# Performance work log

Measured on AMD Instinct MI355X. Metric: run time of the kernel, lower is better.

Reference implementation:

```python
import jax, jax.numpy as jnp
import numpy as np

BN_EPS = 1e-5

def conv1d(x, w, b, pad):
    # x: (B, C_in, L), w: (C_out, C_in, K=4), stride 1
    y = jax.lax.conv_general_dilated(x, w, window_strides=(1,), padding=[(pad, pad)],
                                     dimension_numbers=('NCH', 'OIH', 'NCH'))
    return y + b[None, :, None]

def batchnorm_train(x, g, be):
    # training-mode BN over (N, L) per channel, biased variance (torch semantics)
    m = jnp.mean(x, axis=(0, 2), keepdims=True)
    v = jnp.mean((x - m) ** 2, axis=(0, 2), keepdims=True)
    return (x - m) * jax.lax.rsqrt(v + BN_EPS) * g[None, :, None] + be[None, :, None]

def setup_inputs() -> dict:
    key = jax.random.key(0)
    ks = jax.random.split(key, 12)
    B, T, C_in, E, K = 32, 4096, 12, 256, 1024
    d = {}
    d['x'] = jax.random.normal(ks[0], (B, T, C_in), jnp.float32)
    d['w1'] = jax.random.normal(ks[1], (E, C_in, 4), jnp.float32) * 0.1
    d['b1'] = jax.random.normal(ks[2], (E,), jnp.float32) * 0.1
    d['g1'] = jnp.ones((E,), jnp.float32); d['be1'] = jnp.zeros((E,), jnp.float32)
    d['w2'] = jax.random.normal(ks[3], (E, E, 4), jnp.float32) * 0.05
    d['b2'] = jax.random.normal(ks[4], (E,), jnp.float32) * 0.1
    d['g2'] = jnp.ones((E,), jnp.float32); d['be2'] = jnp.zeros((E,), jnp.float32)
    d['w3'] = jax.random.normal(ks[5], (E, E, 4), jnp.float32) * 0.05
    d['b3'] = jax.random.normal(ks[6], (E,), jnp.float32) * 0.1
    d['g3'] = jnp.ones((E,), jnp.float32); d['be3'] = jnp.zeros((E,), jnp.float32)
    d['w4'] = jax.random.normal(ks[7], (E, E, 4), jnp.float32) * 0.05
    d['b4'] = jax.random.normal(ks[8], (E,), jnp.float32) * 0.1
    d['codebook'] = jax.random.normal(ks[9], (K, E), jnp.float32)
    return d

def reference(x, w1, b1, g1, be1, w2, b2, g2, be2, w3, b3, g3, be3, w4, b4, codebook):
    h = jnp.transpose(x, (0, 2, 1))                 # (B, C, T)
    h = jax.nn.relu(batchnorm_train(conv1d(h, w1, b1, 2), g1, be1))  # (B,E,T+1)
    h = jax.nn.relu(batchnorm_train(conv1d(h, w2, b2, 1), g2, be2))  # (B,E,T)
    h = jax.nn.relu(batchnorm_train(conv1d(h, w3, b3, 2), g3, be3))  # (B,E,T+1)
    h = conv1d(h, w4, b4, 1)                                         # (B,E,T)
    z_e = jnp.transpose(h, (0, 2, 1))               # (B, T, E)
    # squared-L2 nearest codebook entry (argmin identical to cdist p=2)
    d2 = (jnp.sum(z_e ** 2, axis=-1, keepdims=True)
          - 2.0 * jnp.einsum('bte,ke->btk', z_e, codebook)
          + jnp.sum(codebook ** 2, axis=-1)[None, None, :])
    ids = jnp.argmin(d2, axis=-1)                   # (B, T) int
    z_q = codebook[ids]                             # gather (B, T, E)
    z_q = z_e + jax.lax.stop_gradient(z_q - z_e)    # straight-through
    return (z_e, z_q)
```

## Files before the change

kernel.cpp:

```cpp
#include <hip/hip_runtime.h>
#include <hip/hip_bf16.h>


#define B_   32
#define T_   4096
#define E_   256
#define CIN_ 12
#define LM_  4096

typedef __attribute__((ext_vector_type(4))) float f32x4;
typedef __attribute__((ext_vector_type(8))) short bf16x8;
typedef __attribute__((ext_vector_type(8))) unsigned short u16x8;

__device__ __forceinline__ unsigned int bf_rne(float v) {
  unsigned int u = __float_as_uint(v);
  return (u + 0x7fffu + ((u >> 16) & 1u)) >> 16;
}
__device__ __forceinline__ void split2(float v, unsigned short& h, unsigned short& l) {
  unsigned int hu = bf_rne(v);
  h = (unsigned short)hu;
  l = (unsigned short)bf_rne(v - __uint_as_float(hu << 16));
}
__device__ __forceinline__ void split3(float v, unsigned short& a,
                                       unsigned short& b, unsigned short& c) {
  unsigned int h = bf_rne(v);
  a = (unsigned short)h;
  float r1 = v - __uint_as_float(h << 16);
  unsigned int m = bf_rne(r1);
  b = (unsigned short)m;
  float r2 = r1 - __uint_as_float(m << 16);
  c = (unsigned short)bf_rne(r2);
}

__global__ __launch_bounds__(256) void prep_w_kernel(
    const float* __restrict__ w, unsigned short* __restrict__ wh,
    unsigned short* __restrict__ wm, unsigned short* __restrict__ wl) {
  const int g = blockIdx.x * 256 + threadIdx.x;
  const int coff  = g & 31;
  const int e     = (g >> 5) & 255;
  const int slice = g >> 13;
  const int cc = slice >> 2, kt = slice & 3;
  const int c = cc * 32 + coff;
  unsigned short h, m, l;
  split3(w[(size_t)e * 1024 + (size_t)c * 4 + kt], h, m, l);
  const size_t o = (size_t)slice * 8192 + (size_t)e * 32 + coff;
  wh[o] = h; wm[o] = m; wl[o] = l;
}

__global__ __launch_bounds__(256) void conv1_kernel(
    const float* __restrict__ x, const float* __restrict__ w1,
    const float* __restrict__ b1, float* __restrict__ out_main,
    float* __restrict__ out_tail) {
  __shared__ __align__(16) float xs[259][12];
  __shared__ __align__(16) float wsh[E_ * 48];
  __shared__ float bs[E_];
  const int tid = threadIdx.x;
  const int b = blockIdx.y;
  const int l0 = blockIdx.x * 256;
  for (int idx = tid; idx < 259 * 12; idx += 256) {
    int r = idx / 12, c = idx - r * 12;
    int t = l0 - 2 + r;
    xs[r][c] = (t >= 0 && t < T_) ? x[((size_t)b * T_ + t) * CIN_ + c] : 0.f;
  }
  for (int idx = tid; idx < E_ * 48; idx += 256) wsh[idx] = w1[idx];
  bs[tid] = b1[tid];
  __syncthreads();
  float xr[4][12];
  #pragma unroll
  for (int r = 0; r < 4; ++r)
    #pragma unroll
    for (int c = 0; c < 12; ++c) xr[r][c] = xs[tid + r][c];
  const int l = l0 + tid;
  for (int e = 0; e < E_; ++e) {
    float acc = bs[e];
    #pragma unroll
    for (int c = 0; c < 12; ++c) {
      const float4 wv = *(const float4*)&wsh[e * 48 + c * 4];
      acc += wv.x * xr[0][c] + wv.y * xr[1][c] + wv.z * xr[2][c] + wv.w * xr[3][c];
    }
    if (l < LM_)       out_main[((size_t)b * E_ + e) * LM_ + l] = acc;
    else if (l == LM_) out_tail[(size_t)b * E_ + e] = acc;
  }
}

__global__ __launch_bounds__(256) void bn_pass1(
    const float* __restrict__ hmain, const float* __restrict__ htail,
    float* __restrict__ psum, float* __restrict__ psq) {
  const int bx = blockIdx.x;
  const int c = bx >> 3, sl = bx & 7;
  const int tid = threadIdx.x;
  float s = 0.f, s2 = 0.f;
  for (int b = 0; b < B_; ++b) {
    const float* p = hmain + ((size_t)b * E_ + c) * LM_ + sl * 512;
    const float v0 = p[tid], v1 = p[tid + 256];
    s += v0 + v1;
    s2 += v0 * v0 + v1 * v1;
  }
  if (htail && sl == 7 && tid < B_) {
    const float v = htail[(size_t)tid * E_ + c];
    s += v; s2 += v * v;
  }
  __shared__ float sh[256], sh2[256];
  sh[tid] = s; sh2[tid] = s2; __syncthreads();
  for (int off = 128; off > 0; off >>= 1) {
    if (tid < off) { sh[tid] += sh[tid + off]; sh2[tid] += sh2[tid + off]; }
    __syncthreads();
  }
  if (tid == 0) { psum[bx] = sh[0]; psq[bx] = sh2[0]; }
}

__global__ __launch_bounds__(256) void bn_pass2(
    const float* __restrict__ psum, const float* __restrict__ psq,
    const float* __restrict__ g, const float* __restrict__ be,
    float* __restrict__ scale, float* __restrict__ shift, int hasTail) {
  const int c = threadIdx.x;
  double s = 0.0, s2 = 0.0;
  #pragma unroll
  for (int i = 0; i < 8; ++i) { s += psum[c * 8 + i]; s2 += psq[c * 8 + i]; }
  double N = (double)B_ * (double)(LM_ + hasTail);
  double m = s / N, var = s2 / N - m * m;
  double a = (double)g[c] / sqrt(var + 1e-5);
  scale[c] = (float)a;
  shift[c] = (float)((double)be[c] - m * a);
}

template <int MODE>
__global__ __launch_bounds__(256) void conv_mfma(
    const float* __restrict__ in_main, const float* __restrict__ in_tail,
    const unsigned short* __restrict__ wh, const unsigned short* __restrict__ wm,
    const unsigned short* __restrict__ wl, const float* __restrict__ bias,
    const float* __restrict__ scale, const float* __restrict__ shift,
    float* __restrict__ out, float* __restrict__ out_tail, int pad) {
  __shared__ __align__(16) char XhB[68 * 64];
  __shared__ __align__(16) char XmB[68 * 64];
  __shared__ __align__(16) char XlB[68 * 64];
  __shared__ float sc_sh[E_], sf_sh[E_];
  const int tid = threadIdx.x, lane = tid & 63, wv = tid >> 6;
  const int q = lane >> 4, n16 = lane & 15;
  const int b = blockIdx.z, l0 = blockIdx.x * 64;
  const int eB = wv * 64;
  sc_sh[tid] = scale[tid]; sf_sh[tid] = shift[tid];

  f32x4 acc[4][4];
  #pragma unroll
  for (int i = 0; i < 4; ++i)
    #pragma unroll
    for (int j = 0; j < 4; ++j) acc[i][j] = (f32x4){0.f, 0.f, 0.f, 0.f};

  const float* inb = in_main + (size_t)b * E_ * LM_;
  const float* intb = in_tail ? (in_tail + (size_t)b * E_) : nullptr;

  for (int cc = 0; cc < 8; ++cc) {
    __syncthreads();
    for (int idx = tid; idx < 272; idx += 256) {
      const int cp = idx & 15, uq = idx >> 4;
      const int c = cc * 32 + cp * 2;
      const int u0 = uq * 4;
      const int lb = l0 - pad + u0;
      const float* pa = inb + (size_t)c * LM_;
      const float* pb = pa + LM_;
      const float sca = sc_sh[c], sfa = sf_sh[c];
      const float scb = sc_sh[c + 1], sfb = sf_sh[c + 1];
      float fa[4], fb[4];
      if (lb >= 0 && lb + 3 < LM_) {
        const f32x4 va = *(const f32x4*)(pa + lb);
        const f32x4 vb = *(const f32x4*)(pb + lb);
        #pragma unroll
        for (int s = 0; s < 4; ++s) {
          fa[s] = fmaxf(fmaf(va[s], sca, sfa), 0.f);
          fb[s] = fmaxf(fmaf(vb[s], scb, sfb), 0.f);
        }
      } else {
        #pragma unroll
        for (int s = 0; s < 4; ++s) {
          const int l = lb + s;
          float oa = 0.f, ob = 0.f;
          if (l >= 0 && l < LM_) {
            oa = fmaxf(fmaf(pa[l], sca, sfa), 0.f);
            ob = fmaxf(fmaf(pb[l], scb, sfb), 0.f);
          } else if (l == LM_ && intb) {
            oa = fmaxf(fmaf(intb[c], sca, sfa), 0.f);
            ob = fmaxf(fmaf(intb[c + 1], scb, sfb), 0.f);
          }
          fa[s] = oa; fb[s] = ob;
        }
      }
      const int cg = cp >> 2;
      const int cb4 = (cp & 3) * 4;
      #pragma unroll
      for (int s = 0; s < 4; ++s) {
        const int u = u0 + s;
        unsigned short ha, ma, la, hb, mb, lb2;
        split3(fa[s], ha, ma, la);
        split3(fb[s], hb, mb, lb2);
        const int off = u * 64 + ((cg ^ ((u >> 1) & 3)) << 4) + cb4;
        *(unsigned int*)(XhB + off) = (unsigned int)ha | ((unsigned int)hb << 16);
        *(unsigned int*)(XmB + off) = (unsigned int)ma | ((unsigned int)mb << 16);
        *(unsigned int*)(XlB + off) = (unsigned int)la | ((unsigned int)lb2 << 16);
      }
    }
    __syncthreads();
    for (int kt = 0; kt < 4; ++kt) {
      bf16x8 Bh[4], Bm[4], Bl[4];
      #pragma unroll
      for (int ni = 0; ni < 4; ++ni) {
        const int u = ni * 16 + n16 + kt;
        const int off = u * 64 + ((q ^ ((u >> 1) & 3)) << 4);
        Bh[ni] = *(const bf16x8*)(XhB + off);
        Bm[ni] = *(const bf16x8*)(XmB + off);
        Bl[ni] = *(const bf16x8*)(XlB + off);
      }
      const size_t so = (size_t)(cc * 4 + kt) * 8192 + (size_t)q * 8;
      #pragma unroll
      for (int mi = 0; mi < 4; ++mi) {
        const size_t o = so + (size_t)(eB + mi * 16 + n16) * 32;
        const bf16x8 Ah = *(const bf16x8*)(wh + o);
        const bf16x8 Am = *(const bf16x8*)(wm + o);
        const bf16x8 Al = *(const bf16x8*)(wl + o);
        #pragma unroll
        for (int ni = 0; ni < 4; ++ni) {
          acc[mi][ni] = __builtin_amdgcn_mfma_f32_16x16x32_bf16(Ah, Bh[ni], acc[mi][ni], 0, 0, 0);
          acc[mi][ni] = __builtin_amdgcn_mfma_f32_16x16x32_bf16(Ah, Bm[ni], acc[mi][ni], 0, 0, 0);
          acc[mi][ni] = __builtin_amdgcn_mfma_f32_16x16x32_bf16(Am, Bh[ni], acc[mi][ni], 0, 0, 0);
          acc[mi][ni] = __builtin_amdgcn_mfma_f32_16x16x32_bf16(Ah, Bl[ni], acc[mi][ni], 0, 0, 0);
          acc[mi][ni] = __builtin_amdgcn_mfma_f32_16x16x32_bf16(Al, Bh[ni], acc[mi][ni], 0, 0, 0);
          acc[mi][ni] = __builtin_amdgcn_mfma_f32_16x16x32_bf16(Am, Bm[ni], acc[mi][ni], 0, 0, 0);
        }
      }
    }
  }

  #pragma unroll
  for (int mi = 0; mi < 4; ++mi) {
    const int eb4 = eB + mi * 16 + q * 4;
    const f32x4 bv = *(const f32x4*)(bias + eb4);
    #pragma unroll
    for (int ni = 0; ni < 4; ++ni) {
      const int col = l0 + ni * 16 + n16;
      const f32x4 r = acc[mi][ni] + bv;
      if constexpr (MODE == 0) {
        #pragma unroll
        for (int rr = 0; rr < 4; ++rr)
          out[((size_t)b * E_ + eb4 + rr) * LM_ + col] = r[rr];
      } else if constexpr (MODE == 1) {
        if (col < LM_) {
          #pragma unroll
          for (int rr = 0; rr < 4; ++rr)
            out[((size_t)b * E_ + eb4 + rr) * LM_ + col] = r[rr];
        } else if (col == LM_) {
          #pragma unroll
          for (int rr = 0; rr < 4; ++rr)
            out_tail[(size_t)b * E_ + eb4 + rr] = r[rr];
        }
      } else {
        #pragma unroll
        for (int rr = 0; rr < 4; ++rr)
          out[((size_t)b * T_ + col) * E_ + eb4 + rr] = r[rr];
      }
    }
  }
}

__global__ __launch_bounds__(256) void cbprep_kernel(
    const float* __restrict__ cb, unsigned short* __restrict__ cbh,
    unsigned short* __restrict__ cbl, float* __restrict__ cnh) {
  const int code = blockIdx.x * 4 + (threadIdx.x >> 6);
  const int lane = threadIdx.x & 63;
  const f32x4 v = *(const f32x4*)&cb[(size_t)code * E_ + lane * 4];
  ushort4 h, l;
  split2(v.x, h.x, l.x); split2(v.y, h.y, l.y);
  split2(v.z, h.z, l.z); split2(v.w, h.w, l.w);
  *(ushort4*)&cbh[(size_t)code * E_ + lane * 4] = h;
  *(ushort4*)&cbl[(size_t)code * E_ + lane * 4] = l;
  float s = v.x * v.x + v.y * v.y + v.z * v.z + v.w * v.w;
  for (int off = 32; off > 0; off >>= 1) s += __shfl_xor(s, off, 64);
  if (lane == 0) cnh[code] = 0.5f * s;
}

__global__ __launch_bounds__(256) void vq_mfma_kernel(
    const float* __restrict__ z, const unsigned short* __restrict__ cbh,
    const unsigned short* __restrict__ cbl, const float* __restrict__ cnh,
    int* __restrict__ ids) {
  __shared__ __align__(16) char cbLds[2][16384];
  __shared__ float cn_sh[1024];
  const int tid = threadIdx.x;
  const int lane = tid & 63;
  const int w = tid >> 6;
  const int q = lane >> 4;
  const int m15 = lane & 15;
  const int rbase = blockIdx.x * 128 + w * 32;
  for (int i = tid; i < 1024; i += 256) cn_sh[i] = cnh[i];

  const int sc0 = tid >> 5, sl0 = tid & 31;
  const int sc1 = (tid + 256) >> 5, sl1 = (tid + 256) & 31;
  const int d0 = sc0 * 512 + (((sl0 ^ (sc0 & 7))) << 4);
  const int d1 = sc1 * 512 + (((sl1 ^ (sc1 & 7))) << 4);
  const u16x8* srcH = (const u16x8*)cbh;
  const u16x8* srcL = (const u16x8*)cbl;

  {
    u16x8 h0 = srcH[tid], h1 = srcH[tid + 256];
    u16x8 l0 = srcL[tid], l1 = srcL[tid + 256];
    *(u16x8*)(cbLds[0] + d0) = h0;
    *(u16x8*)(cbLds[0] + d1) = h1;
    *(u16x8*)(cbLds[0] + 8192 + d0) = l0;
    *(u16x8*)(cbLds[0] + 8192 + d1) = l1;
  }

  bf16x8 zh[2][8], zl[2][8];
  #pragma unroll
  for (int g = 0; g < 2; ++g) {
    const int row = rbase + g * 16 + m15;
    const float* zr = z + (size_t)row * 256 + q * 8;
    #pragma unroll
    for (int ec = 0; ec < 8; ++ec) {
      const f32x4 v0 = *(const f32x4*)(zr + ec * 32);
      const f32x4 v1 = *(const f32x4*)(zr + ec * 32 + 4);
      u16x8 h, l;
      #pragma unroll
      for (int j = 0; j < 4; ++j) {
        unsigned short a, b;
        split2(v0[j], a, b); h[j] = a; l[j] = b;
        split2(v1[j], a, b); h[4 + j] = a; l[4 + j] = b;
      }
      zh[g][ec] = (bf16x8)h;
      zl[g][ec] = (bf16x8)l;
    }
  }
  __syncthreads();

  float best[2] = {-3.4e38f, -3.4e38f};
  int bidx[2] = {0, 0};
  const int swz = (m15 & 7) << 4;
  const int rowOff = m15 * 512;

  for (int cg = 0; cg < 64; ++cg) {
    const int cur = cg & 1;
    u16x8 ph0, ph1, pl0, pl1;
    if (cg < 63) {
      const int sb = (cg + 1) * 512;
      ph0 = srcH[sb + tid]; ph1 = srcH[sb + tid + 256];
      pl0 = srcL[sb + tid]; pl1 = srcL[sb + tid + 256];
    }
    const char* baseH = cbLds[cur];
    const char* baseL = cbLds[cur] + 8192;
    f32x4 ahh[2], ahl[2], alh[2];
    #pragma unroll
    for (int g = 0; g < 2; ++g) {
      ahh[g] = (f32x4){0.f, 0.f, 0.f, 0.f};
      ahl[g] = (f32x4){0.f, 0.f, 0.f, 0.f};
      alh[g] = (f32x4){0.f, 0.f, 0.f, 0.f};
    }
    #pragma unroll
    for (int ec = 0; ec < 8; ++ec) {
      const int co = rowOff + ((q * 16 + ec * 64) ^ swz);
      const bf16x8 Ah = *(const bf16x8*)(baseH + co);
      const bf16x8 Al = *(const bf16x8*)(baseL + co);
      #pragma unroll
      for (int g = 0; g < 2; ++g) {
        ahh[g] = __builtin_amdgcn_mfma_f32_16x16x32_bf16(Ah, zh[g][ec], ahh[g], 0, 0, 0);
        ahl[g] = __builtin_amdgcn_mfma_f32_16x16x32_bf16(Ah, zl[g][ec], ahl[g], 0, 0, 0);
        alh[g] = __builtin_amdgcn_mfma_f32_16x16x32_bf16(Al, zh[g][ec], alh[g], 0, 0, 0);
      }
    }
    const f32x4 cn = *(const f32x4*)&cn_sh[cg * 16 + q * 4];
    #pragma unroll
    for (int g = 0; g < 2; ++g) {
      #pragma unroll
      for (int r = 0; r < 4; ++r) {
        const float s = (ahh[g][r] + ahl[g][r]) + alh[g][r] - cn[r];
        const int code = cg * 16 + q * 4 + r;
        if (s > best[g]) { best[g] = s; bidx[g] = code; }
      }
    }
    if (cg < 63) {
      char* nb = cbLds[cur ^ 1];
      *(u16x8*)(nb + d0) = ph0;
      *(u16x8*)(nb + d1) = ph1;
      *(u16x8*)(nb + 8192 + d0) = pl0;
      *(u16x8*)(nb + 8192 + d1) = pl1;
    }
    __syncthreads();
  }

  #pragma unroll
  for (int g = 0; g < 2; ++g) {
    #pragma unroll
    for (int off = 16; off <= 32; off <<= 1) {
      const float ov = __shfl_xor(best[g], off, 64);
      const int oi = __shfl_xor(bidx[g], off, 64);
      if (ov > best[g] || (ov == best[g] && oi < bidx[g])) { best[g] = ov; bidx[g] = oi; }
    }
  }
  if (q == 0) {
    #pragma unroll
    for (int g = 0; g < 2; ++g) ids[rbase + g * 16 + lane] = bidx[g];
  }
}

__global__ __launch_bounds__(256) void gather_kernel(
    const int* __restrict__ ids, const float* __restrict__ cb,
    float* __restrict__ zq) {
  const int row = blockIdx.x * 4 + (threadIdx.x >> 6);
  const int lane = threadIdx.x & 63;
  const int id = ids[row];
  const float4 v = *(const float4*)&cb[(size_t)id * E_ + lane * 4];
  *(float4*)&zq[(size_t)row * E_ + lane * 4] = v;
}

extern "C" void kernel_launch(void* const* d_in, const int* in_sizes, int n_in,
                              void* d_out, int out_size, void* d_ws, size_t ws_size,
                              hipStream_t stream) {
  const float* x   = (const float*)d_in[0];
  const float* w1  = (const float*)d_in[1];
  const float* b1  = (const float*)d_in[2];
  const float* g1  = (const float*)d_in[3];
  const float* be1 = (const float*)d_in[4];
  const float* w2  = (const float*)d_in[5];
  const float* b2  = (const float*)d_in[6];
  const float* g2  = (const float*)d_in[7];
  const float* be2 = (const float*)d_in[8];
  const float* w3  = (const float*)d_in[9];
  const float* b3  = (const float*)d_in[10];
  const float* g3  = (const float*)d_in[11];
  const float* be3 = (const float*)d_in[12];
  const float* w4  = (const float*)d_in[13];
  const float* b4  = (const float*)d_in[14];
  const float* cb  = (const float*)d_in[15];

  char* ws = (char*)d_ws;
  float* tailA  = (float*)(ws);
  float* scale1 = (float*)(ws + 40960);  float* shift1 = (float*)(ws + 45056);
  float* scale2 = (float*)(ws + 49152);  float* shift2 = (float*)(ws + 53248);
  float* scale3 = (float*)(ws + 57344);  float* shift3 = (float*)(ws + 61440);
  float* cnh    = (float*)(ws + 65536);
  float* psum   = (float*)(ws + 73728);
  float* psq    = (float*)(ws + 81920);
  int*   ids    = (int*)(ws + 131072);
  const size_t MB = 1u << 20;
  unsigned short* wh2 = (unsigned short*)(ws + MB);
  unsigned short* wm2 = (unsigned short*)(ws + MB + 524288u);
  unsigned short* wl2 = (unsigned short*)(ws + MB + 1048576u);
  unsigned short* wh3 = (unsigned short*)(ws + MB + 1572864u);
  unsigned short* wm3 = (unsigned short*)(ws + MB + 2097152u);
  unsigned short* wl3 = (unsigned short*)(ws + MB + 2621440u);
  unsigned short* wh4 = (unsigned short*)(ws + MB + 3145728u);
  unsigned short* wm4 = (unsigned short*)(ws + MB + 3670016u);
  unsigned short* wl4 = (unsigned short*)(ws + MB + 4194304u);

  float* half1 = (float*)d_out;
  float* half2 = half1 + (size_t)33554432;
  unsigned short* cbh = (unsigned short*)half2;
  unsigned short* cbl = (unsigned short*)half2 + 262144;

  prep_w_kernel<<<1024, 256, 0, stream>>>(w2, wh2, wm2, wl2);
  prep_w_kernel<<<1024, 256, 0, stream>>>(w3, wh3, wm3, wl3);
  prep_w_kernel<<<1024, 256, 0, stream>>>(w4, wh4, wm4, wl4);

  conv1_kernel<<<dim3(17, 32), 256, 0, stream>>>(x, w1, b1, half2, tailA);
  bn_pass1<<<2048, 256, 0, stream>>>(half2, tailA, psum, psq);
  bn_pass2<<<1, 256, 0, stream>>>(psum, psq, g1, be1, scale1, shift1, 1);
  conv_mfma<0><<<dim3(64, 1, 32), 256, 0, stream>>>(half2, tailA, wh2, wm2, wl2, b2,
                                                    scale1, shift1, half1, nullptr, 1);
  bn_pass1<<<2048, 256, 0, stream>>>(half1, nullptr, psum, psq);
  bn_pass2<<<1, 256, 0, stream>>>(psum, psq, g2, be2, scale2, shift2, 0);
  conv_mfma<1><<<dim3(65, 1, 32), 256, 0, stream>>>(half1, nullptr, wh3, wm3, wl3, b3,
                                                    scale2, shift2, half2, tailA, 2);
  bn_pass1<<<2048, 256, 0, stream>>>(half2, tailA, psum, psq);
  bn_pass2<<<1, 256, 0, stream>>>(psum, psq, g3, be3, scale3, shift3, 1);
  conv_mfma<2><<<dim3(64, 1, 32), 256, 0, stream>>>(half2, tailA, wh4, wm4, wl4, b4,
                                                    scale3, shift3, half1, nullptr, 1);
  cbprep_kernel<<<256, 256, 0, stream>>>(cb, cbh, cbl, cnh);
  vq_mfma_kernel<<<1024, 256, 0, stream>>>(half1, cbh, cbl, cnh, ids);
  gather_kernel<<<32768, 256, 0, stream>>>(ids, cb, half2);
}
```

Measured before the change: 1.444 ms.

## Stage two channel chunks per barrier in conv and fuse codebook gather into VQ

The conv kernel now stages 64 input channels (two 32-channel slices) into LDS between barriers instead of 32, halving the number of __syncthreads rounds at the cost of doubled LDS per block. Separately, the VQ argmin kernel now writes z_q directly by broadcasting each winning index via shuffle and copying the codebook row, removing the ids buffer and the separate gather kernel launch. The codebook split buffers move into the workspace, reusing the wh2/wm2 area that is dead by then, because half2 is now written inside the VQ kernel while those buffers are still being read. More LDS use may reduce occupancy.

```diff
diff --git a/kernel.cpp b/kernel.cpp
--- a/kernel.cpp
+++ b/kernel.cpp
@@ -131,9 +131,9 @@
     const unsigned short* __restrict__ wl, const float* __restrict__ bias,
     const float* __restrict__ scale, const float* __restrict__ shift,
     float* __restrict__ out, float* __restrict__ out_tail, int pad) {
-  __shared__ __align__(16) char XhB[68 * 64];
-  __shared__ __align__(16) char XmB[68 * 64];
-  __shared__ __align__(16) char XlB[68 * 64];
+  __shared__ __align__(16) char XhB[2 * 4352];
+  __shared__ __align__(16) char XmB[2 * 4352];
+  __shared__ __align__(16) char XlB[2 * 4352];
   __shared__ float sc_sh[E_], sf_sh[E_];
   const int tid = threadIdx.x, lane = tid & 63, wv = tid >> 6;
   const int q = lane >> 4, n16 = lane & 15;
@@ -150,10 +150,13 @@
   const float* inb = in_main + (size_t)b * E_ * LM_;
   const float* intb = in_tail ? (in_tail + (size_t)b * E_) : nullptr;
 
-  for (int cc = 0; cc < 8; ++cc) {
+  for (int ccp = 0; ccp < 4; ++ccp) {
     __syncthreads();
-    for (int idx = tid; idx < 272; idx += 256) {
-      const int cp = idx & 15, uq = idx >> 4;
+    for (int idx = tid; idx < 544; idx += 256) {
+      const int sl2 = (idx >= 272) ? 1 : 0;
+      const int local = idx - sl2 * 272;
+      const int cp = local & 15, uq = local >> 4;
+      const int cc = ccp * 2 + sl2;
       const int c = cc * 32 + cp * 2;
       const int u0 = uq * 4;
       const int lb = l0 - pad + u0;
@@ -187,44 +190,51 @@
       }
       const int cg = cp >> 2;
       const int cb4 = (cp & 3) * 4;
+      const int sbase = sl2 * 4352;
       #pragma unroll
       for (int s = 0; s < 4; ++s) {
         const int u = u0 + s;
         unsigned short ha, ma, la, hb, mb, lb2;
         split3(fa[s], ha, ma, la);
         split3(fb[s], hb, mb, lb2);
-        const int off = u * 64 + ((cg ^ ((u >> 1) & 3)) << 4) + cb4;
+        const int off = sbase + u * 64 + ((cg ^ ((u >> 1) & 3)) << 4) + cb4;
         *(unsigned int*)(XhB + off) = (unsigned int)ha | ((unsigned int)hb << 16);
         *(unsigned int*)(XmB + off) = (unsigned int)ma | ((unsigned int)mb << 16);
         *(unsigned int*)(XlB + off) = (unsigned int)la | ((unsigned int)lb2 << 16);
       }
     }
     __syncthreads();
-    for (int kt = 0; kt < 4; ++kt) {
-      bf16x8 Bh[4], Bm[4], Bl[4];
-      #pragma unroll
-      for (int ni = 0; ni < 4; ++ni) {
-        const int u = ni * 16 + n16 + kt;
-        const int off = u * 64 + ((q ^ ((u >> 1) & 3)) << 4);
-        Bh[ni] = *(const bf16x8*)(XhB + off);
-        Bm[ni] = *(const bf16x8*)(XmB + off);
-        Bl[ni] = *(const bf16x8*)(XlB + off);
-      }
-      const size_t so = (size_t)(cc * 4 + kt) * 8192 + (size_t)q * 8;
-      #pragma unroll
-      for (int mi = 0; mi < 4; ++mi) {
-        const size_t o = so + (size_t)(eB + mi * 16 + n16) * 32;
-        const bf16x8 Ah = *(const bf16x8*)(wh + o);
-        const bf16x8 Am = *(const bf16x8*)(wm + o);
-        const bf16x8 Al = *(const bf16x8*)(wl + o);
+    for (int sl2 = 0; sl2 < 2; ++sl2) {
+      const int cc = ccp * 2 + sl2;
+      const char* Xh = XhB + sl2 * 4352;
+      const char* Xm = XmB + sl2 * 4352;
+      const char* Xl = XlB + sl2 * 4352;
+      for (int kt = 0; kt < 4; ++kt) {
+        bf16x8 Bh[4], Bm[4], Bl[4];
         #pragma unroll
         for (int ni = 0; ni < 4; ++ni) {
-          acc[mi][ni] = __builtin_amdgcn_mfma_f32_16x16x32_bf16(Ah, Bh[ni], acc[mi][ni], 0, 0, 0);
-          acc[mi][ni] = __builtin_amdgcn_mfma_f32_16x16x32_bf16(Ah, Bm[ni], acc[mi][ni], 0, 0, 0);
-          acc[mi][ni] = __builtin_amdgcn_mfma_f32_16x16x32_bf16(Am, Bh[ni], acc[mi][ni], 0, 0, 0);
-          acc[mi][ni] = __builtin_amdgcn_mfma_f32_16x16x32_bf16(Ah, Bl[ni], acc[mi][ni], 0, 0, 0);
-          acc[mi][ni] = __builtin_amdgcn_mfma_f32_16x16x32_bf16(Al, Bh[ni], acc[mi][ni], 0, 0, 0);
-          acc[mi][ni] = __builtin_amdgcn_mfma_f32_16x16x32_bf16(Am, Bm[ni], acc[mi][ni], 0, 0, 0);
+          const int u = ni * 16 + n16 + kt;
+          const int off = u * 64 + ((q ^ ((u >> 1) & 3)) << 4);
+          Bh[ni] = *(const bf16x8*)(Xh + off);
+          Bm[ni] = *(const bf16x8*)(Xm + off);
+          Bl[ni] = *(const bf16x8*)(Xl + off);
+        }
+        const size_t so = (size_t)(cc * 4 + kt) * 8192 + (size_t)q * 8;
+        #pragma unroll
+        for (int mi = 0; mi < 4; ++mi) {
+          const size_t o = so + (size_t)(eB + mi * 16 + n16) * 32;
+          const bf16x8 Ah = *(const bf16x8*)(wh + o);
+          const bf16x8 Am = *(const bf16x8*)(wm + o);
+          const bf16x8 Al = *(const bf16x8*)(wl + o);
+          #pragma unroll
+          for (int ni = 0; ni < 4; ++ni) {
+            acc[mi][ni] = __builtin_amdgcn_mfma_f32_16x16x32_bf16(Ah, Bh[ni], acc[mi][ni], 0, 0, 0);
+            acc[mi][ni] = __builtin_amdgcn_mfma_f32_16x16x32_bf16(Ah, Bm[ni], acc[mi][ni], 0, 0, 0);
+            acc[mi][ni] = __builtin_amdgcn_mfma_f32_16x16x32_bf16(Am, Bh[ni], acc[mi][ni], 0, 0, 0);
+            acc[mi][ni] = __builtin_amdgcn_mfma_f32_16x16x32_bf16(Ah, Bl[ni], acc[mi][ni], 0, 0, 0);
+            acc[mi][ni] = __builtin_amdgcn_mfma_f32_16x16x32_bf16(Al, Bh[ni], acc[mi][ni], 0, 0, 0);
+            acc[mi][ni] = __builtin_amdgcn_mfma_f32_16x16x32_bf16(Am, Bm[ni], acc[mi][ni], 0, 0, 0);
+          }
         }
       }
     }
@@ -280,7 +290,7 @@
 __global__ __launch_bounds__(256) void vq_mfma_kernel(
     const float* __restrict__ z, const unsigned short* __restrict__ cbh,
     const unsigned short* __restrict__ cbl, const float* __restrict__ cnh,
-    int* __restrict__ ids) {
+    const float* __restrict__ cb, float* __restrict__ zq) {
   __shared__ __align__(16) char cbLds[2][16384];
   __shared__ float cn_sh[1024];
   const int tid = threadIdx.x;
@@ -392,20 +402,15 @@
       if (ov > best[g] || (ov == best[g] && oi < bidx[g])) { best[g] = ov; bidx[g] = oi; }
     }
   }
-  if (q == 0) {
-    #pragma unroll
-    for (int g = 0; g < 2; ++g) ids[rbase + g * 16 + lane] = bidx[g];
-  }
-}
-
-__global__ __launch_bounds__(256) void gather_kernel(
-    const int* __restrict__ ids, const float* __restrict__ cb,
-    float* __restrict__ zq) {
-  const int row = blockIdx.x * 4 + (threadIdx.x >> 6);
-  const int lane = threadIdx.x & 63;
-  const int id = ids[row];
-  const float4 v = *(const float4*)&cb[(size_t)id * E_ + lane * 4];
-  *(float4*)&zq[(size_t)row * E_ + lane * 4] = v;
+  #pragma unroll
+  for (int g = 0; g < 2; ++g) {
+    for (int j = 0; j < 16; ++j) {
+      const int id = __shfl(bidx[g], j, 64);
+      const int row = rbase + g * 16 + j;
+      const f32x4 v = *(const f32x4*)(cb + (size_t)id * 256 + lane * 4);
+      *(f32x4*)(zq + (size_t)row * 256 + lane * 4) = v;
+    }
+  }
 }
 
 extern "C" void kernel_launch(void* const* d_in, const int* in_sizes, int n_in,
@@ -436,7 +441,6 @@
   float* cnh    = (float*)(ws + 65536);
   float* psum   = (float*)(ws + 73728);
   float* psq    = (float*)(ws + 81920);
-  int*   ids    = (int*)(ws + 131072);
   const size_t MB = 1u << 20;
   unsigned short* wh2 = (unsigned short*)(ws + MB);
   unsigned short* wm2 = (unsigned short*)(ws + MB + 524288u);
@@ -447,11 +451,11 @@
   unsigned short* wh4 = (unsigned short*)(ws + MB + 3145728u);
   unsigned short* wm4 = (unsigned short*)(ws + MB + 3670016u);
   unsigned short* wl4 = (unsigned short*)(ws + MB + 4194304u);
+  unsigned short* cbh = (unsigned short*)(ws + MB);
+  unsigned short* cbl = (unsigned short*)(ws + MB + 524288u);
 
   float* half1 = (float*)d_out;
   float* half2 = half1 + (size_t)33554432;
-  unsigned short* cbh = (unsigned short*)half2;
-  unsigned short* cbl = (unsigned short*)half2 + 262144;
 
   prep_w_kernel<<<1024, 256, 0, stream>>>(w2, wh2, wm2, wl2);
   prep_w_kernel<<<1024, 256, 0, stream>>>(w3, wh3, wm3, wl3);
@@ -471,6 +475,5 @@
   conv_mfma<2><<<dim3(64, 1, 32), 256, 0, stream>>>(half2, tailA, wh4, wm4, wl4, b4,
                                                     scale3, shift3, half1, nullptr, 1);
   cbprep_kernel<<<256, 256, 0, stream>>>(cb, cbh, cbl, cnh);
-  vq_mfma_kernel<<<1024, 256, 0, stream>>>(half1, cbh, cbl, cnh, ids);
-  gather_kernel<<<32768, 256, 0, stream>>>(ids, cb, half2);
-}
+  vq_mfma_kernel<<<1024, 256, 0, stream>>>(half1, cbh, cbl, cnh, cb, half2);
+}
```

Measured after the change: 1.486 ms. +3.0%, slower.
